# Optimization experiments

Measured on AMD Instinct MI355X. Metric: run time of the kernel, lower is better.

## Reference

```python
import jax, jax.numpy as jnp
import numpy as np

# ---- config (mirrors init_kwargs) ----
H = 128
W = 128
FMO_STEPS = 4
INPUT_FRAMES = 1
N_PIECES = 1
N_TERMS = 2
CAM_DIST = 2.0
ROT_DIVIDE = 1.0
SIGMAINV = 7000.0
ERODE_K = 5
FOCAL = float(1.0 / np.tan(1.57 / 4.0))  # generate_perspective_projection(1.57/2), aspect=1


def quaternion_to_angle_axis(q):
    # q: [B,4] in (w,x,y,z) convention (torchgeometry)
    q1, q2, q3 = q[..., 1], q[..., 2], q[..., 3]
    sin_sq = q1 * q1 + q2 * q2 + q3 * q3
    sin_t = jnp.sqrt(sin_sq + 1e-20)
    cos_t = q[..., 0]
    two_theta = 2.0 * jnp.where(cos_t < 0.0, jnp.arctan2(-sin_t, -cos_t), jnp.arctan2(sin_t, cos_t))
    k = jnp.where(sin_sq > 1e-12, two_theta / sin_t, 2.0)
    return q[..., 1:4] * k[..., None]


def angle_axis_to_rotation_matrix(aa):
    # aa: [B,3] -> [B,3,3] (Rodrigues)
    th = jnp.sqrt(jnp.sum(aa * aa, axis=-1, keepdims=True) + 1e-12)  # [B,1]
    k = aa / th
    kx, ky, kz = k[..., 0], k[..., 1], k[..., 2]
    zero = jnp.zeros_like(kx)
    K = jnp.stack([jnp.stack([zero, -kz, ky], -1),
                   jnp.stack([kz, zero, -kx], -1),
                   jnp.stack([-ky, kx, zero], -1)], -2)
    s = jnp.sin(th)[..., None]
    c = jnp.cos(th)[..., None]
    return jnp.eye(3, dtype=aa.dtype) + s * K + (1.0 - c) * jnp.matmul(K, K)


def rasterize(fv_img, fv_z, face_feat, fn_z):
    # fv_img [B,F,3,2] NDC, fv_z [B,F,3] camera z, face_feat [B,F,3,C], fn_z [B,F]
    B, F = fv_img.shape[:2]
    xs = jnp.linspace(-1.0, 1.0, W)
    ys = jnp.linspace(1.0, -1.0, H)
    py, px = jnp.meshgrid(ys, xs, indexing='ij')  # [H,W]
    a, b, c = fv_img[:, :, 0], fv_img[:, :, 1], fv_img[:, :, 2]  # [B,F,2]
    e0 = b - a
    e1 = c - a
    denom = e0[..., 0] * e1[..., 1] - e0[..., 1] * e1[..., 0]  # [B,F]
    valid = (fn_z > 0.0) & (jnp.abs(denom) > 1e-10)
    inv_den = jnp.where(jnp.abs(denom) > 1e-10, 1.0 / denom, 0.0)
    dx = px[None, None] - a[..., 0][..., None, None]  # [B,F,H,W]
    dy = py[None, None] - a[..., 1][..., None, None]
    w1 = (dx * e1[..., 1][..., None, None] - dy * e1[..., 0][..., None, None]) * inv_den[..., None, None]
    w2 = (e0[..., 0][..., None, None] * dy - e0[..., 1][..., None, None] * dx) * inv_den[..., None, None]
    w0 = 1.0 - w1 - w2
    inside = (w0 >= 0.0) & (w1 >= 0.0) & (w2 >= 0.0) & valid[..., None, None]
    zi = (w0 * fv_z[:, :, 0, None, None] + w1 * fv_z[:, :, 1, None, None] + w2 * fv_z[:, :, 2, None, None])
    score = jnp.where(inside, zi, -1e10)  # camera looks down -z: nearest face has max z
    best = jnp.argmax(score, axis=1)      # [B,H,W] z-buffer winner
    hit = jnp.any(inside, axis=1)
    bary = jnp.stack([w0, w1, w2], axis=-1)  # [B,F,H,W,3]
    idx = jnp.broadcast_to(best[:, None, :, :, None], (B, 1, H, W, 3))
    bary_b = jnp.take_along_axis(bary, idx, axis=1)[:, 0]  # [B,H,W,3]
    feat_b = jax.vmap(lambda f, i: f[i])(face_feat, best)  # [B,H,W,3,C]
    feats = jnp.einsum('bhwkc,bhwk->bhwc', feat_b, bary_b) * hit[..., None]
    # DIB-R soft silhouette: A = 1 - prod(1 - exp(-sigmainv*d^2)), d = dist to triangle, 0 inside
    d2 = None
    tri = (a, b, c)
    for i in range(3):
        p, q = tri[i], tri[(i + 1) % 3]
        ex = (q - p)[..., 0][..., None, None]
        ey = (q - p)[..., 1][..., None, None]
        rx = px[None, None] - p[..., 0][..., None, None]
        ry = py[None, None] - p[..., 1][..., None, None]
        L2 = ex * ex + ey * ey + 1e-12
        t = jnp.clip((rx * ex + ry * ey) / L2, 0.0, 1.0)
        dxe = rx - t * ex
        dye = ry - t * ey
        dd = dxe * dxe + dye * dye
        d2 = dd if d2 is None else jnp.minimum(d2, dd)
    d2 = jnp.where(inside, 0.0, d2)
    prob = jnp.where(valid[..., None, None], jnp.exp(-SIGMAINV * d2), 0.0)
    mask = 1.0 - jnp.prod(1.0 - prob, axis=1)  # [B,H,W]
    return feats, mask


def texture_sample(tex, uv):
    # tex [B,3,Th,Tw], uv [B,H,W,2] in [0,1]; bilinear, v axis flipped (image row 0 <-> v=1)
    Th, Tw = tex.shape[2], tex.shape[3]
    u = jnp.clip(uv[..., 0], 0.0, 1.0) * (Tw - 1)
    v = (1.0 - jnp.clip(uv[..., 1], 0.0, 1.0)) * (Th - 1)
    x0 = jnp.floor(u)
    y0 = jnp.floor(v)
    fx = (u - x0)[:, None]  # [B,1,H,W]
    fy = (v - y0)[:, None]
    x0i = jnp.clip(x0.astype(jnp.int32), 0, Tw - 1)
    x1i = jnp.clip(x0i + 1, 0, Tw - 1)
    y0i = jnp.clip(y0.astype(jnp.int32), 0, Th - 1)
    y1i = jnp.clip(y0i + 1, 0, Th - 1)
    g = jax.vmap(lambda t, yy, xx: t[:, yy, xx])  # [B,3,H,W]
    t00 = g(tex, y0i, x0i)
    t01 = g(tex, y0i, x1i)
    t10 = g(tex, y1i, x0i)
    t11 = g(tex, y1i, x1i)
    return t00 * (1 - fx) * (1 - fy) + t01 * fx * (1 - fy) + t10 * (1 - fx) * fy + t11 * fx * fy


def erode(m, k):
    # kornia erosion with an all-ones kxk kernel == min-pool (geodesic border)
    return -jax.lax.reduce_window(-m, -jnp.inf, jax.lax.max, (1, k, k), (1, 1, 1), 'SAME')


def render_frame(verts_world, faces, face_features, texture_maps):
    # camera at (0,0,CAM_DIST) looking at origin with up=(0,1,0): R_cam == I
    v_cam = verts_world - jnp.array([0.0, 0.0, CAM_DIST], dtype=verts_world.dtype)
    fv_cam = v_cam[:, faces]  # [B,F,3,3]
    n = jnp.cross(fv_cam[:, :, 1] - fv_cam[:, :, 0], fv_cam[:, :, 2] - fv_cam[:, :, 0])
    n = n / (jnp.linalg.norm(n, axis=-1, keepdims=True) + 1e-10)
    fn_z = n[..., 2]
    z = fv_cam[..., 2]  # negative in front of camera
    img = FOCAL * fv_cam[..., :2] / (-z[..., None] + 1e-10)  # [B,F,3,2]
    uv, mask = rasterize(img, z, face_features, fn_z)
    rgb = texture_sample(texture_maps, uv)  # [B,3,H,W]
    mask_e = erode(mask, ERODE_K)
    return jnp.concatenate([rgb, mask_e[:, None]], axis=1)  # [B,4,H,W]


def reference(vertices, translation, quaternion, exp, face_features, texture_maps, faces):
    rot = angle_axis_to_rotation_matrix(quaternion_to_angle_axis(quaternion[:, 0, 0]))
    trans_start = translation[:, :, 0, 0]  # [B,1,3]
    all_renders = []
    renders = []
    frames = 0
    time_before = 0.0
    for pind in range(N_PIECES):
        angles = quaternion_to_angle_axis(quaternion[:, pind, 1]) / ROT_DIVIDE
        rot_step = angle_axis_to_rotation_matrix(exp * angles / FMO_STEPS)
        rot_noexp = angle_axis_to_rotation_matrix(angles * (1.0 - exp))
        n_steps = FMO_STEPS * INPUT_FRAMES // N_PIECES  # prop[pind] (forced for single piece)
        for ti in np.linspace(0.0, 1.0, n_steps):
            if frames == 0:
                time_before = ti
            time_exp = time_before + (ti - time_before) * exp  # [1]
            verts = jnp.einsum('bij,bvj->bvi', rot, vertices) + trans_start
            for p in range(1, N_TERMS):
                verts = verts + (time_exp ** p) * translation[:, :, pind, p]
            renders.append(render_frame(verts, faces, face_features, texture_maps))
            frames += 1
            if frames == FMO_STEPS:
                frames = 0
                all_renders.append(jnp.stack(renders, 1))
                renders = []
                rot = jnp.matmul(rot, rot_noexp)
            else:
                rot = jnp.matmul(rot, rot_step)
        for p in range(1, N_TERMS):
            trans_start = trans_start + translation[:, :, pind, p]
    return jnp.stack(all_renders, 1)  # [B, input_frames, fmo_steps, 4, H, W]


def setup_inputs() -> dict:
    key = jax.random.key(0)
    ks = jax.random.split(key, 7)
    B, V, F = 1, 162, 320
    vertices = jax.random.normal(ks[0], (B, V, 3), jnp.float32) * 0.3
    translation = jax.random.normal(ks[1], (B, 1, N_PIECES, N_TERMS, 3), jnp.float32) * 0.1
    quaternion = jax.random.normal(ks[2], (B, N_PIECES, 2, 4), jnp.float32)
    exp = jax.random.uniform(ks[3], (1,), jnp.float32)
    face_features = jax.random.uniform(ks[4], (B, F, 3, 2), jnp.float32)
    texture_maps = jax.random.uniform(ks[5], (B, 3, 256, 256), jnp.float32)
    faces = jax.random.randint(ks[6], (F, 3), 0, V)
    return {"vertices": vertices, "translation": translation, "quaternion": quaternion,
            "exp": exp, "face_features": face_features, "texture_maps": texture_maps,
            "faces": faces}
```

## Files before the change

### kernel.cpp

```cpp
#include <hip/hip_runtime.h>
#include <math.h>

#define N_FRAMES 4
#define N_FACES  320
#define N_VERTS  162
#define IMG_H    128
#define IMG_W    128
#define NWAVES   8
#define FPW      40
#define REC_SZ   20

#define SV_OFF   0
#define BB_OFF   1952
#define BB_LD    48
#define REC_OFF  8096
#define ARENA_SZ 33696



__device__ __forceinline__ void q_to_aa(const float* q, float* aa) {
    float q1 = q[1], q2 = q[2], q3 = q[3];
    float sin_sq = (q1 * q1 + q2 * q2) + q3 * q3;
    float sin_t = sqrtf(sin_sq + 1e-20f);
    float cos_t = q[0];
    float two_theta = (cos_t < 0.0f) ? (2.0f * atan2f(-sin_t, -cos_t))
                                     : (2.0f * atan2f(sin_t, cos_t));
    float k = (sin_sq > 1e-12f) ? (two_theta / sin_t) : 2.0f;
    aa[0] = q1 * k; aa[1] = q2 * k; aa[2] = q3 * k;
}

__device__ __forceinline__ void aa_to_R(const float* aa, float* R) {
    float th = sqrtf(((aa[0] * aa[0] + aa[1] * aa[1]) + aa[2] * aa[2]) + 1e-12f);
    float kx = aa[0] / th, ky = aa[1] / th, kz = aa[2] / th;
    float K[9] = { 0.0f, -kz,  ky,
                   kz,  0.0f, -kx,
                  -ky,   kx, 0.0f };
    float s = sinf(th), c = cosf(th);
    float KK[9];
    for (int i = 0; i < 3; ++i)
        for (int j = 0; j < 3; ++j)
            KK[i*3+j] = (K[i*3+0] * K[0*3+j] + K[i*3+1] * K[1*3+j]) + K[i*3+2] * K[2*3+j];
    float omc = 1.0f - c;
    for (int i = 0; i < 9; ++i) {
        float eye = (i == 0 || i == 4 || i == 8) ? 1.0f : 0.0f;
        R[i] = (eye + s * K[i]) + omc * KK[i];
    }
}

__device__ __forceinline__ void mat3mul(const float* A, const float* B, float* C) {
    for (int i = 0; i < 3; ++i)
        for (int j = 0; j < 3; ++j)
            C[i*3+j] = (A[i*3+0] * B[0*3+j] + A[i*3+1] * B[1*3+j]) + A[i*3+2] * B[2*3+j];
}


__global__ void __launch_bounds__(512)
render_kernel(const float* __restrict__ verts_in,
              const float* __restrict__ transl,
              const float* __restrict__ quat,
              const float* __restrict__ expv,
              const int*   __restrict__ faces,
              const float* __restrict__ ffeat,
              const float* __restrict__ tex,
              float* __restrict__ out,
              float* __restrict__ maskbuf)
{
    __shared__ __align__(16) char arena[ARENA_SZ];
    float* sv   = (float*)(arena + SV_OFF);
    float* bb   = (float*)(arena + BB_OFF);
    float* recs = (float*)(arena + REC_OFF);
    float* red  = (float*)arena;

    int frame = blockIdx.x >> 8;
    int blk   = blockIdx.x & 255;
    int tid   = threadIdx.x;
    int lane  = tid & 63;
    int wv    = __builtin_amdgcn_readfirstlane(tid >> 6);
    int tile_x = blk & 7, tile_y = blk >> 3;
    int j = tile_x * 16 + (lane & 15);
    int i = tile_y * 4 + (lane >> 4);

    float e = expv[0];
    float R[9];
    {
        float aa0[3], aa1[3], S[9];
        q_to_aa(quat, aa0);
        aa_to_R(aa0, R);
        q_to_aa(quat + 4, aa1);
        float arg[3];
        for (int t = 0; t < 3; ++t) arg[t] = (e * aa1[t]) / 4.0f;
        aa_to_R(arg, S);
        for (int t = 0; t < frame; ++t) {
            float nxt[9];
            mat3mul(R, S, nxt);
            for (int q = 0; q < 9; ++q) R[q] = nxt[q];
        }
    }

    if (tid < N_VERTS) {
        float te = (float)((double)frame / 3.0) * e;
        float vx = verts_in[tid*3+0], vy = verts_in[tid*3+1], vz = verts_in[tid*3+2];
        float dx_ = (R[0] * vx + R[1] * vy) + R[2] * vz;
        float dy_ = (R[3] * vx + R[4] * vy) + R[5] * vz;
        float dz_ = (R[6] * vx + R[7] * vy) + R[8] * vz;
        float x = (dx_ + transl[0]) + te * transl[3];
        float y = (dy_ + transl[1]) + te * transl[4];
        float z = (dz_ + transl[2]) + te * transl[5];
        z = z - 2.0f;
        sv[tid*3+0] = x; sv[tid*3+1] = y; sv[tid*3+2] = z;
    }
    __syncthreads();

    const float FOCAL = (float)(1.0 / tan(1.57 / 4.0));
    int cnt;
    {
        bool valid = false;
        float ax=0, ay=0, bx=0, by=0, cx=0, cy=0, e0x=0, e0y=0, e1x=0, e1y=0;
        float e12x=0, e12y=0, z0=0, z1=0, z2=0, den=0;
        int f = wv * FPW + lane;
        if (lane < FPW) {
            int i0 = faces[f*3+0], i1 = faces[f*3+1], i2 = faces[f*3+2];
            const float* A = &sv[i0*3];
            const float* B = &sv[i1*3];
            const float* C = &sv[i2*3];
            float ux = B[0] - A[0], uy = B[1] - A[1];
            float wx = C[0] - A[0], wy = C[1] - A[1];
            float nz = ux * wy - uy * wx;
            float da = -A[2] + 1e-10f, db = -B[2] + 1e-10f, dc = -C[2] + 1e-10f;
            ax = (FOCAL * A[0]) / da; ay = (FOCAL * A[1]) / da;
            bx = (FOCAL * B[0]) / db; by = (FOCAL * B[1]) / db;
            cx = (FOCAL * C[0]) / dc; cy = (FOCAL * C[1]) / dc;
            e0x = bx - ax; e0y = by - ay;
            e1x = cx - ax; e1y = cy - ay;
            e12x = cx - bx; e12y = cy - by;
            den = e0x * e1y - e0y * e1x;
            z0 = A[2]; z1 = B[2]; z2 = C[2];
            valid = (fabsf(den) > 1e-10f) && (nz > 0.0f);
        }
        unsigned long long m = __ballot(valid);
        cnt = __popcll(m);
        if (valid) {
            unsigned long long lmask = (lane == 63) ? 0x7fffffffffffffffull
                                                    : ((1ull << lane) - 1ull);
            int pos = __popcll(m & lmask);
            float invden = 1.0f / den;
            float L2_0 = (e0x * e0x + e0y * e0y) + 1e-12f;
            float L2_1 = (e12x * e12x + e12y * e12y) + 1e-12f;
            float L2_2 = (e1x * e1x + e1y * e1y) + 1e-12f;
            float4* r = (float4*)&recs[(wv * FPW + pos) * REC_SZ];
            r[0] = make_float4(ax, ay, e0x, e0y);
            r[1] = make_float4(e1x, e1y, invden, (float)f);
            r[2] = make_float4(z0, z1, z2, 1.0f / L2_0);
            r[3] = make_float4(bx, by, e12x, e12y);
            r[4] = make_float4(cx, cy, 1.0f / L2_1, 1.0f / L2_2);
            float* wbb = &bb[wv * 4 * BB_LD];
            wbb[0*BB_LD + pos] = fminf(fminf(ax, bx), cx);
            wbb[1*BB_LD + pos] = fminf(fminf(ay, by), cy);
            wbb[2*BB_LD + pos] = fmaxf(fmaxf(ax, bx), cx);
            wbb[3*BB_LD + pos] = fmaxf(fmaxf(ay, by), cy);
        }
    }

    float px = (float)(-1.0 + 2.0 * (double)j / 127.0);
    float py = (float)( 1.0 - 2.0 * (double)i / 127.0);
    float txmin = (float)(-1.0 + 2.0 * (double)(tile_x * 16) / 127.0);
    float txmax = (float)(-1.0 + 2.0 * (double)(tile_x * 16 + 15) / 127.0);
    float tymax = (float)( 1.0 - 2.0 * (double)(tile_y * 4) / 127.0);
    float tymin = (float)( 1.0 - 2.0 * (double)(tile_y * 4 + 3) / 127.0);

    unsigned long long fmask;
    {
        int l = (lane < FPW) ? lane : 0;
        const float* wbb = &bb[wv * 4 * BB_LD];
        float xmin = wbb[0*BB_LD + l], ymin = wbb[1*BB_LD + l];
        float xmax = wbb[2*BB_LD + l], ymax = wbb[3*BB_LD + l];
        float cdx = fmaxf(fmaxf(xmin - txmax, txmin - xmax), 0.0f);
        float cdy = fmaxf(fmaxf(ymin - tymax, tymin - ymax), 0.0f);
        bool near = ((cdx * cdx + cdy * cdy) <= 0.0026f) && (lane < cnt);
        fmask = __ballot(near);
    }

    float best = -1e10f;
    int bestf = 0;
    float bw0 = 0.0f, bw1 = 0.0f, bw2 = 0.0f;
    float P = 1.0f;

    while (fmask) {
        int fc = __ffsll((unsigned long long)fmask) - 1;
        fmask &= fmask - 1;
        const float* d = &recs[(wv * FPW + fc) * REC_SZ];

        float ax = d[0], ay = d[1], e0x = d[2], e0y = d[3];
        float e1x = d[4], e1y = d[5], invden = d[6], fidx = d[7];
        float z0 = d[8], z1 = d[9], z2 = d[10], invL2_0 = d[11];
        float bx = d[12], by = d[13], e12x = d[14], e12y = d[15];
        float cx = d[16], cy = d[17], invL2_1 = d[18], invL2_2 = d[19];

        float dx = px - ax, dy = py - ay;
        float w1 = (dx * e1y - dy * e1x) * invden;
        float w2 = (e0x * dy - e0y * dx) * invden;
        float w0 = (1.0f - w1) - w2;
        bool inside = (w0 >= 0.0f) & (w1 >= 0.0f) & (w2 >= 0.0f);
        float zi = (w0 * z0 + w1 * z1) + w2 * z2;
        float score = inside ? zi : -1e10f;
        if (score > best) {
            best = score; bestf = (int)fidx; bw0 = w0; bw1 = w1; bw2 = w2;
        }

        float t0 = fminf(fmaxf((dx * e0x + dy * e0y) * invL2_0, 0.0f), 1.0f);
        float x0 = dx - t0 * e0x, y0 = dy - t0 * e0y;
        float dd = x0 * x0 + y0 * y0;
        float rx1 = px - bx, ry1 = py - by;
        float t1 = fminf(fmaxf((rx1 * e12x + ry1 * e12y) * invL2_1, 0.0f), 1.0f);
        float x1 = rx1 - t1 * e12x, y1 = ry1 - t1 * e12y;
        dd = fminf(dd, x1 * x1 + y1 * y1);
        float ex2 = -e1x, ey2 = -e1y;
        float rx2 = px - cx, ry2 = py - cy;
        float t2 = fminf(fmaxf((rx2 * ex2 + ry2 * ey2) * invL2_2, 0.0f), 1.0f);
        float x2 = rx2 - t2 * ex2, y2 = ry2 - t2 * ey2;
        dd = fminf(dd, x2 * x2 + y2 * y2);

        float d2 = inside ? 0.0f : dd;
        float prob = __expf(-7000.0f * d2);
        P *= (1.0f - prob);
    }

    __syncthreads();
    float* my = &red[tid * 6];
    my[0] = best; my[1] = __int_as_float(bestf);
    my[2] = bw0;  my[3] = bw1; my[4] = bw2; my[5] = P;
    __syncthreads();

    if (tid < 64) {
        float bbst = red[tid * 6 + 0];
        int   bf   = __float_as_int(red[tid * 6 + 1]);
        float r0 = red[tid * 6 + 2], r1 = red[tid * 6 + 3], r2 = red[tid * 6 + 4];
        float Pt = red[tid * 6 + 5];
        for (int w = 1; w < NWAVES; ++w) {
            const float* s = &red[(w * 64 + tid) * 6];
            float sc = s[0]; int ff = __float_as_int(s[1]);
            if ((sc > bbst) || ((sc == bbst) && (ff < bf))) {
                bbst = sc; bf = ff; r0 = s[2]; r1 = s[3]; r2 = s[4];
            }
            Pt *= s[5];
        }

        bool hit = bbst != -1e10f;
        float uv0 = 0.0f, uv1 = 0.0f;
        if (hit) {
            const float* fp = ffeat + bf * 6;
            uv0 = (fp[0] * r0 + fp[2] * r1) + fp[4] * r2;
            uv1 = (fp[1] * r0 + fp[3] * r1) + fp[5] * r2;
        }
        float u = fminf(fmaxf(uv0, 0.0f), 1.0f) * 255.0f;
        float v = (1.0f - fminf(fmaxf(uv1, 0.0f), 1.0f)) * 255.0f;
        float x0f = floorf(u), y0f = floorf(v);
        float fx = u - x0f, fy = v - y0f;
        int x0i = min(max((int)x0f, 0), 255);
        int x1i = min(x0i + 1, 255);
        int y0i = min(max((int)y0f, 0), 255);
        int y1i = min(y0i + 1, 255);

        for (int c = 0; c < 3; ++c) {
            const float* tc = tex + c * 65536;
            float t00 = tc[y0i * 256 + x0i];
            float t01 = tc[y0i * 256 + x1i];
            float t10 = tc[y1i * 256 + x0i];
            float t11 = tc[y1i * 256 + x1i];
            float val = (t00 * (1.0f - fx)) * (1.0f - fy);
            val = val + (t01 * fx) * (1.0f - fy);
            val = val + (t10 * (1.0f - fx)) * fy;
            val = val + (t11 * fx) * fy;
            out[((frame * 4 + c) * IMG_H + i) * IMG_W + j] = val;
        }
        maskbuf[(frame * IMG_H + i) * IMG_W + j] = 1.0f - Pt;
    }
}


__global__ void __launch_bounds__(256)
erode_kernel(const float* __restrict__ maskbuf, float* __restrict__ out)
{
    int frame = blockIdx.x >> 6;
    int pix = (blockIdx.x & 63) * 256 + threadIdx.x;
    int i = pix >> 7, j = pix & 127;
    float m = 1e30f;
    for (int di = -2; di <= 2; ++di) {
        int ii = i + di;
        if (ii < 0 || ii >= IMG_H) continue;
        for (int dj = -2; dj <= 2; ++dj) {
            int jj = j + dj;
            if (jj < 0 || jj >= IMG_W) continue;
            m = fminf(m, maskbuf[(frame * IMG_H + ii) * IMG_W + jj]);
        }
    }
    out[((frame * 4 + 3) * IMG_H + i) * IMG_W + j] = m;
}


extern "C" void kernel_launch(void* const* d_in, const int* in_sizes, int n_in,
                              void* d_out, int out_size, void* d_ws, size_t ws_size,
                              hipStream_t stream) {
    const float* vertices      = (const float*)d_in[0];
    const float* translation   = (const float*)d_in[1];
    const float* quaternion    = (const float*)d_in[2];
    const float* expv          = (const float*)d_in[3];
    const float* face_features = (const float*)d_in[4];
    const float* texture_maps  = (const float*)d_in[5];
    const int*   faces         = (const int*)d_in[6];
    float* out = (float*)d_out;

    float* maskbuf = (float*)d_ws;

    render_kernel<<<N_FRAMES * 256, 512, 0, stream>>>(vertices, translation,
                                                      quaternion, expv, faces,
                                                      face_features, texture_maps,
                                                      out, maskbuf);
    erode_kernel<<<N_FRAMES * 64, 256, 0, stream>>>(maskbuf, out);
}
```

Measured before the change: 90.15 us.

## Fuse erosion into render kernel by computing soft mask on halo tile

```diff
diff --git a/kernel.cpp b/kernel.cpp
--- a/kernel.cpp
+++ b/kernel.cpp
@@ -9,12 +9,18 @@
 #define NWAVES   8
 #define FPW      40
 #define REC_SZ   20
+#define HW       20
+#define HH       8
+#define HN       (HW * HH)
 
 #define SV_OFF   0
 #define BB_OFF   1952
 #define BB_LD    48
 #define REC_OFF  8096
 #define ARENA_SZ 33696
+#define RED_OFF  0
+#define PB_OFF   12288
+#define MK_OFF   18048
 
 
 
@@ -53,6 +59,34 @@
             C[i*3+j] = (A[i*3+0] * B[0*3+j] + A[i*3+1] * B[1*3+j]) + A[i*3+2] * B[2*3+j];
 }
 
+__device__ __forceinline__ float face_factor(float px, float py, const float* d) {
+    float ax = d[0], ay = d[1], e0x = d[2], e0y = d[3];
+    float e1x = d[4], e1y = d[5], invden = d[6];
+    float invL2_0 = d[11];
+    float bx = d[12], by = d[13], e12x = d[14], e12y = d[15];
+    float cx = d[16], cy = d[17], invL2_1 = d[18], invL2_2 = d[19];
+
+    float dx = px - ax, dy = py - ay;
+    float w1 = (dx * e1y - dy * e1x) * invden;
+    float w2 = (e0x * dy - e0y * dx) * invden;
+    float w0 = (1.0f - w1) - w2;
+    bool inside = (w0 >= 0.0f) & (w1 >= 0.0f) & (w2 >= 0.0f);
+    float t0 = fminf(fmaxf((dx * e0x + dy * e0y) * invL2_0, 0.0f), 1.0f);
+    float x0 = dx - t0 * e0x, y0 = dy - t0 * e0y;
+    float dd = x0 * x0 + y0 * y0;
+    float rx1 = px - bx, ry1 = py - by;
+    float t1 = fminf(fmaxf((rx1 * e12x + ry1 * e12y) * invL2_1, 0.0f), 1.0f);
+    float x1 = rx1 - t1 * e12x, y1 = ry1 - t1 * e12y;
+    dd = fminf(dd, x1 * x1 + y1 * y1);
+    float ex2 = -e1x, ey2 = -e1y;
+    float rx2 = px - cx, ry2 = py - cy;
+    float t2 = fminf(fmaxf((rx2 * ex2 + ry2 * ey2) * invL2_2, 0.0f), 1.0f);
+    float x2 = rx2 - t2 * ex2, y2 = ry2 - t2 * ey2;
+    dd = fminf(dd, x2 * x2 + y2 * y2);
+    float d2 = inside ? 0.0f : dd;
+    return 1.0f - __expf(-7000.0f * d2);
+}
+
 
 __global__ void __launch_bounds__(512)
 render_kernel(const float* __restrict__ verts_in,
@@ -62,14 +96,15 @@
               const int*   __restrict__ faces,
               const float* __restrict__ ffeat,
               const float* __restrict__ tex,
-              float* __restrict__ out,
-              float* __restrict__ maskbuf)
+              float* __restrict__ out)
 {
     __shared__ __align__(16) char arena[ARENA_SZ];
     float* sv   = (float*)(arena + SV_OFF);
     float* bb   = (float*)(arena + BB_OFF);
     float* recs = (float*)(arena + REC_OFF);
-    float* red  = (float*)arena;
+    float* red  = (float*)(arena + RED_OFF);
+    float* Pbuf = (float*)(arena + PB_OFF);
+    float* mk   = (float*)(arena + MK_OFF);
 
     int frame = blockIdx.x >> 8;
     int blk   = blockIdx.x & 255;
@@ -163,13 +198,27 @@
 
     float px = (float)(-1.0 + 2.0 * (double)j / 127.0);
     float py = (float)( 1.0 - 2.0 * (double)i / 127.0);
-    float txmin = (float)(-1.0 + 2.0 * (double)(tile_x * 16) / 127.0);
-    float txmax = (float)(-1.0 + 2.0 * (double)(tile_x * 16 + 15) / 127.0);
-    float tymax = (float)( 1.0 - 2.0 * (double)(tile_y * 4) / 127.0);
-    float tymin = (float)( 1.0 - 2.0 * (double)(tile_y * 4 + 3) / 127.0);
+
+    float hpx[3], hpy[3];
+    bool  hin[3];
+    float Ph[3] = {1.0f, 1.0f, 1.0f};
+    #pragma unroll
+    for (int k = 0; k < 3; ++k) {
+        int h = lane + 64 * k;
+        int hy = h / HW, hx = h - hy * HW;
+        int ii = tile_y * 4 - 2 + hy;
+        int jj = tile_x * 16 - 2 + hx;
+        hin[k] = (h < HN) && (ii >= 0) && (ii < IMG_H) && (jj >= 0) && (jj < IMG_W);
+        hpx[k] = (float)(-1.0 + 2.0 * (double)jj / 127.0);
+        hpy[k] = (float)( 1.0 - 2.0 * (double)ii / 127.0);
+    }
 
     unsigned long long fmask;
     {
+        float txmin = (float)(-1.0 + 2.0 * (double)(tile_x * 16 - 2) / 127.0);
+        float txmax = (float)(-1.0 + 2.0 * (double)(tile_x * 16 + 17) / 127.0);
+        float tymax = (float)( 1.0 - 2.0 * (double)(tile_y * 4 - 2) / 127.0);
+        float tymin = (float)( 1.0 - 2.0 * (double)(tile_y * 4 + 5) / 127.0);
         int l = (lane < FPW) ? lane : 0;
         const float* wbb = &bb[wv * 4 * BB_LD];
         float xmin = wbb[0*BB_LD + l], ymin = wbb[1*BB_LD + l];
@@ -183,66 +232,67 @@
     float best = -1e10f;
     int bestf = 0;
     float bw0 = 0.0f, bw1 = 0.0f, bw2 = 0.0f;
-    float P = 1.0f;
 
     while (fmask) {
         int fc = __ffsll((unsigned long long)fmask) - 1;
         fmask &= fmask - 1;
         const float* d = &recs[(wv * FPW + fc) * REC_SZ];
 
-        float ax = d[0], ay = d[1], e0x = d[2], e0y = d[3];
-        float e1x = d[4], e1y = d[5], invden = d[6], fidx = d[7];
-        float z0 = d[8], z1 = d[9], z2 = d[10], invL2_0 = d[11];
-        float bx = d[12], by = d[13], e12x = d[14], e12y = d[15];
-        float cx = d[16], cy = d[17], invL2_1 = d[18], invL2_2 = d[19];
-
-        float dx = px - ax, dy = py - ay;
-        float w1 = (dx * e1y - dy * e1x) * invden;
-        float w2 = (e0x * dy - e0y * dx) * invden;
-        float w0 = (1.0f - w1) - w2;
-        bool inside = (w0 >= 0.0f) & (w1 >= 0.0f) & (w2 >= 0.0f);
-        float zi = (w0 * z0 + w1 * z1) + w2 * z2;
-        float score = inside ? zi : -1e10f;
-        if (score > best) {
-            best = score; bestf = (int)fidx; bw0 = w0; bw1 = w1; bw2 = w2;
-        }
-
-        float t0 = fminf(fmaxf((dx * e0x + dy * e0y) * invL2_0, 0.0f), 1.0f);
-        float x0 = dx - t0 * e0x, y0 = dy - t0 * e0y;
-        float dd = x0 * x0 + y0 * y0;
-        float rx1 = px - bx, ry1 = py - by;
-        float t1 = fminf(fmaxf((rx1 * e12x + ry1 * e12y) * invL2_1, 0.0f), 1.0f);
-        float x1 = rx1 - t1 * e12x, y1 = ry1 - t1 * e12y;
-        dd = fminf(dd, x1 * x1 + y1 * y1);
-        float ex2 = -e1x, ey2 = -e1y;
-        float rx2 = px - cx, ry2 = py - cy;
-        float t2 = fminf(fmaxf((rx2 * ex2 + ry2 * ey2) * invL2_2, 0.0f), 1.0f);
-        float x2 = rx2 - t2 * ex2, y2 = ry2 - t2 * ey2;
-        dd = fminf(dd, x2 * x2 + y2 * y2);
-
-        float d2 = inside ? 0.0f : dd;
-        float prob = __expf(-7000.0f * d2);
-        P *= (1.0f - prob);
+        {
+            float dx = px - d[0], dy = py - d[1];
+            float w1 = (dx * d[5] - dy * d[4]) * d[6];
+            float w2 = (d[2] * dy - d[3] * dx) * d[6];
+            float w0 = (1.0f - w1) - w2;
+            bool inside = (w0 >= 0.0f) & (w1 >= 0.0f) & (w2 >= 0.0f);
+            float zi = (w0 * d[8] + w1 * d[9]) + w2 * d[10];
+            float score = inside ? zi : -1e10f;
+            if (score > best) {
+                best = score; bestf = (int)d[7]; bw0 = w0; bw1 = w1; bw2 = w2;
+            }
+        }
+        #pragma unroll
+        for (int k = 0; k < 3; ++k)
+            if (hin[k]) Ph[k] *= face_factor(hpx[k], hpy[k], d);
     }
 
     __syncthreads();
-    float* my = &red[tid * 6];
-    my[0] = best; my[1] = __int_as_float(bestf);
-    my[2] = bw0;  my[3] = bw1; my[4] = bw2; my[5] = P;
+    {
+        float* my = &red[tid * 6];
+        my[0] = best; my[1] = __int_as_float(bestf);
+        my[2] = bw0;  my[3] = bw1; my[4] = bw2; my[5] = 0.0f;
+        #pragma unroll
+        for (int k = 0; k < 3; ++k) {
+            int h = lane + 64 * k;
+            if (h < HN) Pbuf[h * 9 + wv] = Ph[k];
+        }
+    }
+    __syncthreads();
+
+    if (tid < HN) {
+        int hy = tid / HW, hx = tid - hy * HW;
+        int ii = tile_y * 4 - 2 + hy;
+        int jj = tile_x * 16 - 2 + hx;
+        bool inb = (ii >= 0) && (ii < IMG_H) && (jj >= 0) && (jj < IMG_W);
+        if (inb) {
+            float Pt = Pbuf[tid * 9 + 0];
+            for (int w = 1; w < NWAVES; ++w) Pt *= Pbuf[tid * 9 + w];
+            mk[tid] = 1.0f - Pt;
+        } else {
+            mk[tid] = 1e30f;
+        }
+    }
     __syncthreads();
 
     if (tid < 64) {
         float bbst = red[tid * 6 + 0];
         int   bf   = __float_as_int(red[tid * 6 + 1]);
         float r0 = red[tid * 6 + 2], r1 = red[tid * 6 + 3], r2 = red[tid * 6 + 4];
-        float Pt = red[tid * 6 + 5];
         for (int w = 1; w < NWAVES; ++w) {
             const float* s = &red[(w * 64 + tid) * 6];
             float sc = s[0]; int ff = __float_as_int(s[1]);
             if ((sc > bbst) || ((sc == bbst) && (ff < bf))) {
                 bbst = sc; bf = ff; r0 = s[2]; r1 = s[3]; r2 = s[4];
             }
-            Pt *= s[5];
         }
 
         bool hit = bbst != -1e10f;
@@ -273,28 +323,16 @@
             val = val + (t11 * fx) * fy;
             out[((frame * 4 + c) * IMG_H + i) * IMG_W + j] = val;
         }
-        maskbuf[(frame * IMG_H + i) * IMG_W + j] = 1.0f - Pt;
-    }
-}
-
-
-__global__ void __launch_bounds__(256)
-erode_kernel(const float* __restrict__ maskbuf, float* __restrict__ out)
-{
-    int frame = blockIdx.x >> 6;
-    int pix = (blockIdx.x & 63) * 256 + threadIdx.x;
-    int i = pix >> 7, j = pix & 127;
-    float m = 1e30f;
-    for (int di = -2; di <= 2; ++di) {
-        int ii = i + di;
-        if (ii < 0 || ii >= IMG_H) continue;
-        for (int dj = -2; dj <= 2; ++dj) {
-            int jj = j + dj;
-            if (jj < 0 || jj >= IMG_W) continue;
-            m = fminf(m, maskbuf[(frame * IMG_H + ii) * IMG_W + jj]);
-        }
-    }
-    out[((frame * 4 + 3) * IMG_H + i) * IMG_W + j] = m;
+
+        int ly = tid >> 4, lx = tid & 15;
+        float m = 1e30f;
+        #pragma unroll
+        for (int di = 0; di < 5; ++di)
+            #pragma unroll
+            for (int dj = 0; dj < 5; ++dj)
+                m = fminf(m, mk[(ly + di) * HW + (lx + dj)]);
+        out[((frame * 4 + 3) * IMG_H + i) * IMG_W + j] = m;
+    }
 }
 
 
@@ -310,11 +348,8 @@
     const int*   faces         = (const int*)d_in[6];
     float* out = (float*)d_out;
 
-    float* maskbuf = (float*)d_ws;
-
     render_kernel<<<N_FRAMES * 256, 512, 0, stream>>>(vertices, translation,
                                                       quaternion, expv, faces,
                                                       face_features, texture_maps,
-                                                      out, maskbuf);
-    erode_kernel<<<N_FRAMES * 64, 256, 0, stream>>>(maskbuf, out);
-}
+                                                      out);
+}
```

After: 107.7 us. 1.19x slower.
